# Performance work log

Measured on AMD Instinct MI355X. Metric: run time of the kernel, lower is better.

## Reference

```python
import jax, jax.numpy as jnp
import numpy as np


def _greedy_match(d):
    # d: [S, S] pairwise distances. Greedy bipartite match: repeatedly take
    # global argmin, record pred_row -> gt_col, mask out that row and column.
    S = d.shape[0]

    def body(i, carry):
        dm, matches = carry
        m = jnp.argmin(dm.reshape(-1))
        r = m // S
        c = m % S
        matches = matches.at[r].set(c)
        dm = dm.at[r, :].set(jnp.inf)
        dm = dm.at[:, c].set(jnp.inf)
        return dm, matches

    _, matches = jax.lax.fori_loop(0, S, body, (d, jnp.zeros((S,), jnp.int32)))
    return matches


def setup_inputs() -> dict:
    key = jax.random.key(0)
    k1, k2 = jax.random.split(key)
    bs, seq_len, n_sources, input_dim = 8, 4096, 4, 257
    predictions = jax.random.normal(k1, (bs, seq_len, n_sources, input_dim), jnp.float32)
    ground_truths = jax.random.normal(k2, (bs, seq_len, n_sources, input_dim), jnp.float32)
    return {"predictions": predictions, "ground_truths": ground_truths}


def reference(predictions, ground_truths):
    # predictions, ground_truths: [bs, seq_len, S, D]
    bs, seq_len, S, D = predictions.shape
    # Flatten each source's full time-frequency signal: [bs, S, seq_len*D]
    p = jnp.transpose(predictions, (0, 2, 1, 3)).reshape(bs, S, seq_len * D)
    g = jnp.transpose(ground_truths, (0, 2, 1, 3)).reshape(bs, S, seq_len * D)

    # Euclidean cdist between pred sources and gt sources: [bs, S, S]
    d2 = (jnp.sum(p * p, axis=-1)[:, :, None]
          + jnp.sum(g * g, axis=-1)[:, None, :]
          - 2.0 * jnp.einsum('bsk,btk->bst', p, g))
    dists = jnp.sqrt(jnp.maximum(d2, 0.0))

    # Greedy assignment (ranks are monotone in distance, so matching on the
    # distances directly is identical to matching on the argsort-rank matrix).
    matches = jax.vmap(_greedy_match)(jax.lax.stop_gradient(dists))  # [bs, S] int32

    # Per-(batch, pred-source) distance to its matched gt source:
    # torch.norm(pred[b] - gt_match[b]) == euclidean dist of flattened vectors.
    gm = jnp.take_along_axis(g, matches[:, :, None], axis=1)  # [bs, S, seq_len*D]
    per = jnp.linalg.norm(p - gm, axis=-1)  # [bs, S]

    return jnp.sum(per) / bs
```

## Files before the change

### kernel.cpp

```cpp
#include <hip/hip_runtime.h>
#include <math.h>

#define BS 8
#define T  4096
#define S  4
#define D  257
#define SD (S * D)
#define K  (T * D)
#define NACC 24

__global__ __launch_bounds__(256) void zero_ws_kernel(float* ws) {
    int i = blockIdx.x * blockDim.x + threadIdx.x;
    if (i < BS * NACC) ws[i] = 0.0f;
}

__global__ __launch_bounds__(256) void partial_kernel(const float* __restrict__ P,
                                                      const float* __restrict__ G,
                                                      float* __restrict__ ws) {
    const int b    = blockIdx.x & 7;
    const int blk  = blockIdx.x >> 3;
    const int nblk = gridDim.x >> 3;
    const int stride = nblk * blockDim.x;

    const float* __restrict__ Pb = P + (size_t)b * T * SD;
    const float* __restrict__ Gb = G + (size_t)b * T * SD;

    float pp0 = 0.f, pp1 = 0.f, pp2 = 0.f, pp3 = 0.f;
    float gg0 = 0.f, gg1 = 0.f, gg2 = 0.f, gg3 = 0.f;
    float pg00=0.f, pg01=0.f, pg02=0.f, pg03=0.f;
    float pg10=0.f, pg11=0.f, pg12=0.f, pg13=0.f;
    float pg20=0.f, pg21=0.f, pg22=0.f, pg23=0.f;
    float pg30=0.f, pg31=0.f, pg32=0.f, pg33=0.f;

    for (int i = blk * blockDim.x + threadIdx.x; i < K; i += stride) {
        int t = i / D;
        int d = i - t * D;
        const float* p = Pb + (size_t)t * SD + d;
        const float* g = Gb + (size_t)t * SD + d;
        float p0 = p[0], p1 = p[D], p2 = p[2*D], p3 = p[3*D];
        float g0 = g[0], g1 = g[D], g2 = g[2*D], g3 = g[3*D];

        pp0 = fmaf(p0, p0, pp0); pp1 = fmaf(p1, p1, pp1);
        pp2 = fmaf(p2, p2, pp2); pp3 = fmaf(p3, p3, pp3);
        gg0 = fmaf(g0, g0, gg0); gg1 = fmaf(g1, g1, gg1);
        gg2 = fmaf(g2, g2, gg2); gg3 = fmaf(g3, g3, gg3);

        pg00 = fmaf(p0, g0, pg00); pg01 = fmaf(p0, g1, pg01);
        pg02 = fmaf(p0, g2, pg02); pg03 = fmaf(p0, g3, pg03);
        pg10 = fmaf(p1, g0, pg10); pg11 = fmaf(p1, g1, pg11);
        pg12 = fmaf(p1, g2, pg12); pg13 = fmaf(p1, g3, pg13);
        pg20 = fmaf(p2, g0, pg20); pg21 = fmaf(p2, g1, pg21);
        pg22 = fmaf(p2, g2, pg22); pg23 = fmaf(p2, g3, pg23);
        pg30 = fmaf(p3, g0, pg30); pg31 = fmaf(p3, g1, pg31);
        pg32 = fmaf(p3, g2, pg32); pg33 = fmaf(p3, g3, pg33);
    }

    float vals[NACC] = { pp0, pp1, pp2, pp3, gg0, gg1, gg2, gg3,
                         pg00, pg01, pg02, pg03,
                         pg10, pg11, pg12, pg13,
                         pg20, pg21, pg22, pg23,
                         pg30, pg31, pg32, pg33 };

    const int lane = threadIdx.x & 63;
    const int wave = threadIdx.x >> 6;
    __shared__ float sm[4][NACC];

    #pragma unroll
    for (int k = 0; k < NACC; ++k) {
        float v = vals[k];
        #pragma unroll
        for (int o = 32; o > 0; o >>= 1) v += __shfl_down(v, o, 64);
        if (lane == 0) sm[wave][k] = v;
    }
    __syncthreads();
    if (threadIdx.x < NACC) {
        float v = sm[0][threadIdx.x] + sm[1][threadIdx.x]
                + sm[2][threadIdx.x] + sm[3][threadIdx.x];
        atomicAdd(&ws[b * NACC + threadIdx.x], v);
    }
}

__global__ void finalize_kernel(const float* __restrict__ ws, float* __restrict__ out) {
    if (threadIdx.x != 0 || blockIdx.x != 0) return;
    float total = 0.f;
    for (int b = 0; b < BS; ++b) {
        const float* w = ws + b * NACC;
        float dist[16];
        for (int s = 0; s < 4; ++s)
            for (int t = 0; t < 4; ++t) {
                float d2 = w[s] + w[4 + t] - 2.f * w[8 + s * 4 + t];
                dist[s * 4 + t] = sqrtf(fmaxf(d2, 0.f));
            }
        bool rdone[4] = {false, false, false, false};
        bool cdone[4] = {false, false, false, false};
        for (int it = 0; it < 4; ++it) {
            float best = INFINITY; int br = 0, bc = 0;
            bool found = false;
            for (int s = 0; s < 4; ++s) {
                if (rdone[s]) continue;
                for (int t = 0; t < 4; ++t) {
                    if (cdone[t]) continue;
                    float v = dist[s * 4 + t];
                    if (!found || v < best) { best = v; br = s; bc = t; found = true; }
                }
            }
            total += best;
            rdone[br] = true; cdone[bc] = true;
        }
    }
    *out = total * 0.125f;
}

extern "C" void kernel_launch(void* const* d_in, const int* in_sizes, int n_in,
                              void* d_out, int out_size, void* d_ws, size_t ws_size,
                              hipStream_t stream) {
    const float* P = (const float*)d_in[0];
    const float* G = (const float*)d_in[1];
    float* out = (float*)d_out;
    float* ws  = (float*)d_ws;

    zero_ws_kernel<<<1, 256, 0, stream>>>(ws);
    partial_kernel<<<2048, 256, 0, stream>>>(P, G, ws);
    finalize_kernel<<<1, 64, 0, stream>>>(ws, out);
}
```

Measured before the change: 74.79 us.

## Stage row tiles into LDS via direct global-to-LDS loads

The kernel now copies contiguous 4-row tiles of P and G into shared memory with 16-byte global_load_lds instructions, then computes the 24 dot-product accumulators from LDS. This replaces the strided per-element global loads. The grid is also changed to 128 blocks per batch, each processing 8 tiles. There is no double buffering, so every tile waits on a full barrier between load and compute, and fewer blocks are resident to hide memory latency.

After: 76.19 us. About the same (+1.9%).

```diff
diff --git a/kernel.cpp b/kernel.cpp
--- a/kernel.cpp
+++ b/kernel.cpp
@@ -3,10 +3,15 @@
 
 #define BS 8
 #define T  4096
-#define S  4
 #define D  257
-#define SD (S * D)
-#define K  (T * D)
+#define SD 1028
+#define ROWS 4
+#define TILE_FLOATS (ROWS * SD)
+#define TILE_BYTES  (TILE_FLOATS * 4)
+#define FULL_CHUNKS 16
+#define TAIL_LANES  4
+#define BPB 128
+#define TILES_PER_BLOCK 8
 #define NACC 24
 
 __global__ __launch_bounds__(256) void zero_ws_kernel(float* ws) {
@@ -14,69 +19,91 @@
     if (i < BS * NACC) ws[i] = 0.0f;
 }
 
+__device__ __forceinline__ void gload16(const float* g, float* l) {
+    __builtin_amdgcn_global_load_lds(
+        (const __attribute__((address_space(1))) unsigned int*)g,
+        (__attribute__((address_space(3))) unsigned int*)l,
+        16, 0, 0);
+}
+
 __global__ __launch_bounds__(256) void partial_kernel(const float* __restrict__ P,
                                                       const float* __restrict__ G,
                                                       float* __restrict__ ws) {
-    const int b    = blockIdx.x & 7;
-    const int blk  = blockIdx.x >> 3;
-    const int nblk = gridDim.x >> 3;
-    const int stride = nblk * blockDim.x;
+    __shared__ float ldsP[TILE_FLOATS];
+    __shared__ float ldsG[TILE_FLOATS];
+    __shared__ float sm[4][NACC];
+
+    const int tid  = threadIdx.x;
+    const int lane = tid & 63;
+    const int wv   = tid >> 6;
+    const int b    = blockIdx.x >> 7;
+    const int blkb = blockIdx.x & (BPB - 1);
 
     const float* __restrict__ Pb = P + (size_t)b * T * SD;
     const float* __restrict__ Gb = G + (size_t)b * T * SD;
 
-    float pp0 = 0.f, pp1 = 0.f, pp2 = 0.f, pp3 = 0.f;
-    float gg0 = 0.f, gg1 = 0.f, gg2 = 0.f, gg3 = 0.f;
-    float pg00=0.f, pg01=0.f, pg02=0.f, pg03=0.f;
-    float pg10=0.f, pg11=0.f, pg12=0.f, pg13=0.f;
-    float pg20=0.f, pg21=0.f, pg22=0.f, pg23=0.f;
-    float pg30=0.f, pg31=0.f, pg32=0.f, pg33=0.f;
+    float acc[NACC];
+    #pragma unroll
+    for (int k = 0; k < NACC; ++k) acc[k] = 0.0f;
 
-    for (int i = blk * blockDim.x + threadIdx.x; i < K; i += stride) {
-        int t = i / D;
-        int d = i - t * D;
-        const float* p = Pb + (size_t)t * SD + d;
-        const float* g = Gb + (size_t)t * SD + d;
-        float p0 = p[0], p1 = p[D], p2 = p[2*D], p3 = p[3*D];
-        float g0 = g[0], g1 = g[D], g2 = g[2*D], g3 = g[3*D];
+    for (int it = 0; it < TILES_PER_BLOCK; ++it) {
+        const int rg = blkb + it * BPB;
+        const float* srcP = Pb + (size_t)rg * TILE_FLOATS;
+        const float* srcG = Gb + (size_t)rg * TILE_FLOATS;
 
-        pp0 = fmaf(p0, p0, pp0); pp1 = fmaf(p1, p1, pp1);
-        pp2 = fmaf(p2, p2, pp2); pp3 = fmaf(p3, p3, pp3);
-        gg0 = fmaf(g0, g0, gg0); gg1 = fmaf(g1, g1, gg1);
-        gg2 = fmaf(g2, g2, gg2); gg3 = fmaf(g3, g3, gg3);
+        #pragma unroll
+        for (int c = 0; c < 4; ++c) {
+            const int off = (wv * 4 + c) * 256;
+            gload16(srcP + off + lane * 4, &ldsP[off]);
+            gload16(srcG + off + lane * 4, &ldsG[off]);
+        }
+        if (wv == 0 && lane < TAIL_LANES)
+            gload16(srcP + FULL_CHUNKS * 256 + lane * 4, &ldsP[FULL_CHUNKS * 256]);
+        if (wv == 1 && lane < TAIL_LANES)
+            gload16(srcG + FULL_CHUNKS * 256 + lane * 4, &ldsG[FULL_CHUNKS * 256]);
+        __syncthreads();
 
-        pg00 = fmaf(p0, g0, pg00); pg01 = fmaf(p0, g1, pg01);
-        pg02 = fmaf(p0, g2, pg02); pg03 = fmaf(p0, g3, pg03);
-        pg10 = fmaf(p1, g0, pg10); pg11 = fmaf(p1, g1, pg11);
-        pg12 = fmaf(p1, g2, pg12); pg13 = fmaf(p1, g3, pg13);
-        pg20 = fmaf(p2, g0, pg20); pg21 = fmaf(p2, g1, pg21);
-        pg22 = fmaf(p2, g2, pg22); pg23 = fmaf(p2, g3, pg23);
-        pg30 = fmaf(p3, g0, pg30); pg31 = fmaf(p3, g1, pg31);
-        pg32 = fmaf(p3, g2, pg32); pg33 = fmaf(p3, g3, pg33);
+        for (int pos = tid; pos < ROWS * D; pos += 256) {
+            const int row = pos / D;
+            const int d   = pos - row * D;
+            const int base = row * SD + d;
+            const float p0 = ldsP[base];
+            const float p1 = ldsP[base + D];
+            const float p2 = ldsP[base + 2 * D];
+            const float p3 = ldsP[base + 3 * D];
+            const float g0 = ldsG[base];
+            const float g1 = ldsG[base + D];
+            const float g2 = ldsG[base + 2 * D];
+            const float g3 = ldsG[base + 3 * D];
+
+            acc[0] = fmaf(p0, p0, acc[0]);  acc[1] = fmaf(p1, p1, acc[1]);
+            acc[2] = fmaf(p2, p2, acc[2]);  acc[3] = fmaf(p3, p3, acc[3]);
+            acc[4] = fmaf(g0, g0, acc[4]);  acc[5] = fmaf(g1, g1, acc[5]);
+            acc[6] = fmaf(g2, g2, acc[6]);  acc[7] = fmaf(g3, g3, acc[7]);
+
+            acc[ 8] = fmaf(p0, g0, acc[ 8]); acc[ 9] = fmaf(p0, g1, acc[ 9]);
+            acc[10] = fmaf(p0, g2, acc[10]); acc[11] = fmaf(p0, g3, acc[11]);
+            acc[12] = fmaf(p1, g0, acc[12]); acc[13] = fmaf(p1, g1, acc[13]);
+            acc[14] = fmaf(p1, g2, acc[14]); acc[15] = fmaf(p1, g3, acc[15]);
+            acc[16] = fmaf(p2, g0, acc[16]); acc[17] = fmaf(p2, g1, acc[17]);
+            acc[18] = fmaf(p2, g2, acc[18]); acc[19] = fmaf(p2, g3, acc[19]);
+            acc[20] = fmaf(p3, g0, acc[20]); acc[21] = fmaf(p3, g1, acc[21]);
+            acc[22] = fmaf(p3, g2, acc[22]); acc[23] = fmaf(p3, g3, acc[23]);
+        }
+        __syncthreads();
     }
-
-    float vals[NACC] = { pp0, pp1, pp2, pp3, gg0, gg1, gg2, gg3,
-                         pg00, pg01, pg02, pg03,
-                         pg10, pg11, pg12, pg13,
-                         pg20, pg21, pg22, pg23,
-                         pg30, pg31, pg32, pg33 };
-
-    const int lane = threadIdx.x & 63;
-    const int wave = threadIdx.x >> 6;
-    __shared__ float sm[4][NACC];
 
     #pragma unroll
     for (int k = 0; k < NACC; ++k) {
-        float v = vals[k];
+        float v = acc[k];
         #pragma unroll
         for (int o = 32; o > 0; o >>= 1) v += __shfl_down(v, o, 64);
-        if (lane == 0) sm[wave][k] = v;
+        if (lane == 0) sm[wv][k] = v;
     }
     __syncthreads();
-    if (threadIdx.x < NACC) {
-        float v = sm[0][threadIdx.x] + sm[1][threadIdx.x]
-                + sm[2][threadIdx.x] + sm[3][threadIdx.x];
-        atomicAdd(&ws[b * NACC + threadIdx.x], v);
+    if (tid < NACC) {
+        float v = sm[0][tid] + sm[1][tid] + sm[2][tid] + sm[3][tid];
+        atomicAdd(&ws[b * NACC + tid], v);
     }
 }
 
@@ -120,6 +147,6 @@
     float* ws  = (float*)d_ws;
 
     zero_ws_kernel<<<1, 256, 0, stream>>>(ws);
-    partial_kernel<<<2048, 256, 0, stream>>>(P, G, ws);
+    partial_kernel<<<BS * BPB, 256, 0, stream>>>(P, G, ws);
     finalize_kernel<<<1, 64, 0, stream>>>(ws, out);
 }
```
